# Kernel optimization log

Measured on AMD Instinct MI355X. Metric: run time of the kernel, lower is better.

## Reference

```python
import jax, jax.numpy as jnp
import numpy as np

N = 100000   # num_nodes
E = 3200000  # num_edges (avg degree 32)
T = 16       # channels
L = 2        # n_layers


def setup_inputs() -> dict:
    key = jax.random.key(0)
    ks = jax.random.split(key, 6)
    x = jax.random.normal(ks[0], (T, N), dtype=jnp.float32)
    edge_index = jax.random.randint(ks[1], (2, E), 0, N)
    # per-layer scalar params (shared='all' -> shape [1,1] each), init U(-1,1)
    alpha1 = jax.random.uniform(ks[2], (L, 1, 1), minval=-1.0, maxval=1.0, dtype=jnp.float32)
    alpha2 = jax.random.uniform(ks[3], (L, 1, 1), minval=-1.0, maxval=1.0, dtype=jnp.float32)
    gamma = jax.random.uniform(ks[4], (L, 1, 1), minval=-1.0, maxval=1.0, dtype=jnp.float32)
    bias = jax.random.uniform(ks[5], (L, 1, 1), minval=-1.0, maxval=1.0, dtype=jnp.float32)
    return {"x": x, "edge_index": edge_index, "alpha1": alpha1,
            "alpha2": alpha2, "gamma": gamma, "bias": bias}


def reference(x, edge_index, alpha1, alpha2, gamma, bias):
    # DGMRF forward (transpose=False, with_bias=True): stack of L DGMRFLayerMultiChannel
    src, dst = edge_index[0], edge_index[1]
    # degrees = ptg.utils.degree(edge_index[0]) (out-degree of source nodes)
    deg = jax.ops.segment_sum(jnp.ones(E, dtype=x.dtype), src, num_segments=N)
    log_deg = jnp.log(deg)[None, :]          # [1, N]
    edge_log_deg = log_deg[0, dst][None, :]  # [1, E] = log_degrees[edge_index[1]] (non-transpose)
    for l in range(L):
        dp = jax.nn.sigmoid(gamma[l])        # degree_power, [1,1]
        sw = jnp.exp(alpha1[l])              # self_weight
        # NOTE: source's alpha2 property returns alpha1_param when shared != 'dynamics'
        nw = sw * jnp.tanh(alpha1[l])        # neighbor_weight
        weighted_repr = x * jnp.exp(dp * log_deg)        # [T, N]
        ew = jnp.exp((dp - 1.0) * edge_log_deg)          # [1, E] (base edge_weights are ones)
        msg = x[:, src] * ew                              # gather + weight: [T, E]
        agg = jnp.zeros_like(x).at[:, dst].add(msg)       # scatter-add aggregate
        x = sw * weighted_repr + nw * agg + bias[l]
    return x
```

## Files before the change

kernel.cpp:

```cpp
#include <hip/hip_runtime.h>


#define TCH 16
#define BBITS 8
#define BINW (1 << BBITS)
#define BLK 256
#define SPILL_CAP 65536

__global__ void k_hist(const int* __restrict__ src, const int* __restrict__ dst,
                       int* __restrict__ Hd, int* __restrict__ Hs,
                       int E, int NB, int CHUNK) {
    extern __shared__ int sm[];
    int* cd = sm; int* cs2 = sm + NB;
    for (int i = threadIdx.x; i < 2 * NB; i += blockDim.x) sm[i] = 0;
    __syncthreads();
    int beg = blockIdx.x * CHUNK;
    int end = beg + CHUNK; if (end > E) end = E;
    for (int i = beg + threadIdx.x; i < end; i += blockDim.x) {
        atomicAdd(&cd[dst[i] >> BBITS], 1);
        atomicAdd(&cs2[src[i] >> BBITS], 1);
    }
    __syncthreads();
    int* hd = Hd + (size_t)blockIdx.x * NB;
    int* hs = Hs + (size_t)blockIdx.x * NB;
    for (int b = threadIdx.x; b < NB; b += blockDim.x) { hd[b] = cd[b]; hs[b] = cs2[b]; }
}

__global__ void k_scanb(const int* __restrict__ H, int* __restrict__ off,
                        int* __restrict__ cnt, int NB, int NBLK) {
    __shared__ int ss[BLK];
    int bin = blockIdx.x;
    int t = threadIdx.x;
    int v[4];
    int sum = 0;
#pragma unroll
    for (int j = 0; j < 4; ++j) {
        int b = t * 4 + j;
        v[j] = (b < NBLK) ? H[(size_t)b * NB + bin] : 0;
        sum += v[j];
    }
    ss[t] = sum;
    __syncthreads();
    for (int o = 1; o < BLK; o <<= 1) {
        int u = (t >= o) ? ss[t - o] : 0;
        __syncthreads();
        ss[t] += u;
        __syncthreads();
    }
    int base = ss[t] - sum;
#pragma unroll
    for (int j = 0; j < 4; ++j) {
        int b = t * 4 + j;
        if (b < NBLK) off[(size_t)b * NB + bin] = base;
        base += v[j];
    }
    if (t == BLK - 1) cnt[bin] = ss[BLK - 1];
}

__global__ __launch_bounds__(BLK) void k_place(
        const int* __restrict__ src, const int* __restrict__ dst,
        const int* __restrict__ offd, const int* __restrict__ offs,
        int* __restrict__ dpairs, unsigned char* __restrict__ srcb,
        int* __restrict__ spill_cnt, int* __restrict__ spill_d,
        int* __restrict__ spill_s,
        int E, int NB, int CHUNK, int CAPB) {
    __shared__ int ss[BLK];
    extern __shared__ int sm[];
    int* cur = sm;
    int* gdl = sm + NB;
    int* pay = sm + 2 * NB;
    int* ga  = sm + 2 * NB + CHUNK;

    int t = threadIdx.x;
    int beg = blockIdx.x * CHUNK;
    int end = beg + CHUNK; if (end > E) end = E;
    int m = end - beg;

    for (int i = t; i < NB; i += BLK) cur[i] = 0;
    __syncthreads();
    for (int i = beg + t; i < end; i += BLK)
        atomicAdd(&cur[dst[i] >> BBITS], 1);
    __syncthreads();
    int c0 = (2 * t     < NB) ? cur[2 * t]     : 0;
    int c1 = (2 * t + 1 < NB) ? cur[2 * t + 1] : 0;
    ss[t] = c0 + c1;
    __syncthreads();
    for (int o = 1; o < BLK; o <<= 1) {
        int v = (t >= o) ? ss[t - o] : 0;
        __syncthreads();
        ss[t] += v;
        __syncthreads();
    }
    int excl = ss[t] - (c0 + c1);
    __syncthreads();
    if (2 * t < NB) {
        int od = offd[(size_t)blockIdx.x * NB + 2 * t];
        cur[2 * t] = excl;
        gdl[2 * t] = 2 * t * CAPB + od - excl;
    }
    if (2 * t + 1 < NB) {
        int od = offd[(size_t)blockIdx.x * NB + 2 * t + 1];
        cur[2 * t + 1] = excl + c0;
        gdl[2 * t + 1] = (2 * t + 1) * CAPB + od - (excl + c0);
    }
    __syncthreads();
    for (int i = beg + t; i < end; i += BLK) {
        int d = dst[i], s = src[i];
        int bd = d >> BBITS;
        int ls = atomicAdd(&cur[bd], 1);
        int g  = gdl[bd] + ls;
        if (g < (bd + 1) * CAPB) {
            pay[ls] = ((d & (BINW - 1)) << 24) | s;
            ga[ls] = g;
        } else {
            ga[ls] = -1;
            int p = atomicAdd(&spill_cnt[0], 1);
            if (p < SPILL_CAP) { spill_d[2 * p] = d; spill_d[2 * p + 1] = s; }
        }
    }
    __syncthreads();
    for (int i = t; i < m; i += BLK) {
        int g = ga[i];
        if (g >= 0) dpairs[g] = pay[i];
    }
    __syncthreads();

    unsigned char* payb = (unsigned char*)pay;
    for (int i = t; i < NB; i += BLK) cur[i] = 0;
    __syncthreads();
    for (int i = beg + t; i < end; i += BLK)
        atomicAdd(&cur[src[i] >> BBITS], 1);
    __syncthreads();
    c0 = (2 * t     < NB) ? cur[2 * t]     : 0;
    c1 = (2 * t + 1 < NB) ? cur[2 * t + 1] : 0;
    ss[t] = c0 + c1;
    __syncthreads();
    for (int o = 1; o < BLK; o <<= 1) {
        int v = (t >= o) ? ss[t - o] : 0;
        __syncthreads();
        ss[t] += v;
        __syncthreads();
    }
    excl = ss[t] - (c0 + c1);
    __syncthreads();
    if (2 * t < NB) {
        int os_ = offs[(size_t)blockIdx.x * NB + 2 * t];
        cur[2 * t] = excl;
        gdl[2 * t] = 2 * t * CAPB + os_ - excl;
    }
    if (2 * t + 1 < NB) {
        int os_ = offs[(size_t)blockIdx.x * NB + 2 * t + 1];
        cur[2 * t + 1] = excl + c0;
        gdl[2 * t + 1] = (2 * t + 1) * CAPB + os_ - (excl + c0);
    }
    __syncthreads();
    for (int i = beg + t; i < end; i += BLK) {
        int s = src[i];
        int bs = s >> BBITS;
        int ls = atomicAdd(&cur[bs], 1);
        int g  = gdl[bs] + ls;
        if (g < (bs + 1) * CAPB) {
            payb[ls] = (unsigned char)(s & (BINW - 1));
            ga[ls] = g;
        } else {
            ga[ls] = -1;
            int p = atomicAdd(&spill_cnt[1], 1);
            if (p < SPILL_CAP) spill_s[p] = s;
        }
    }
    __syncthreads();
    for (int i = t; i < m; i += BLK) {
        int g = ga[i];
        if (g >= 0) srcb[g] = payb[i];
    }
}

__global__ void k_binsort(const int* __restrict__ dpairs, const int* __restrict__ cntd,
                          const unsigned char* __restrict__ srcb, const int* __restrict__ cnts,
                          int* __restrict__ adj, int* __restrict__ rptr,
                          int* __restrict__ rcnt, int* __restrict__ deg,
                          int N, int CAPB) {
    __shared__ int h[BINW];
    __shared__ int o[BINW];
    __shared__ int rk[BINW];
    __shared__ int hd[BINW];
    int bin = blockIdx.x;
    int t = threadIdx.x;
    h[t] = 0; rk[t] = 0; hd[t] = 0;
    __syncthreads();
    int m = cntd[bin]; if (m > CAPB) m = CAPB;
    const int* pp = dpairs + (size_t)bin * CAPB;
    for (int i = t; i < m; i += blockDim.x)
        atomicAdd(&h[((unsigned)pp[i]) >> 24], 1);
    int ms = cnts[bin]; if (ms > CAPB) ms = CAPB;
    const unsigned char* sp = srcb + (size_t)bin * CAPB;
    for (int i = t; i < ms; i += blockDim.x)
        atomicAdd(&hd[sp[i]], 1);
    __syncthreads();
    o[t] = h[t];
    __syncthreads();
    for (int s = 1; s < BINW; s <<= 1) {
        int v = 0;
        if (t >= s) v = o[t - s];
        __syncthreads();
        if (t >= s) o[t] += v;
        __syncthreads();
    }
    int binbase = bin * CAPB;
    {
        int excl = o[t] - h[t];
        o[t] = excl;
        int n = (bin << BBITS) + t;
        if (n < N) { rptr[n] = binbase + excl; rcnt[n] = h[t]; deg[n] = hd[t]; }
    }
    __syncthreads();
    for (int i = t; i < m; i += blockDim.x) {
        int w = pp[i];
        int dl = ((unsigned)w) >> 24;
        int s  = w & 0xFFFFFF;
        int r = atomicAdd(&rk[dl], 1);
        adj[binbase + o[dl] + r] = s;
    }
}

__global__ void k_deg_spill(const int* __restrict__ spill_cnt, const int* __restrict__ spill_s,
                            int* __restrict__ deg) {
    int total = spill_cnt[1]; if (total > SPILL_CAP) total = SPILL_CAP;
    int stride = gridDim.x * blockDim.x;
    for (int i = blockIdx.x * blockDim.x + threadIdx.x; i < total; i += stride)
        atomicAdd(&deg[spill_s[i]], 1);
}

__global__ void k_tin(const float* __restrict__ x, float* __restrict__ xt, int N) {
    int n = blockIdx.x * blockDim.x + threadIdx.x;
    if (n >= N) return;
    float v[TCH];
#pragma unroll
    for (int t = 0; t < TCH; ++t) v[t] = x[(size_t)t * N + n];
    float4* o = reinterpret_cast<float4*>(xt + (size_t)n * TCH);
    o[0] = make_float4(v[0],  v[1],  v[2],  v[3]);
    o[1] = make_float4(v[4],  v[5],  v[6],  v[7]);
    o[2] = make_float4(v[8],  v[9],  v[10], v[11]);
    o[3] = make_float4(v[12], v[13], v[14], v[15]);
}

__global__ void k_layer(const float* __restrict__ xin, float* __restrict__ xout,
                        const int* __restrict__ rptr, const int* __restrict__ rcnt,
                        const int* __restrict__ adj, const int* __restrict__ deg,
                        const float* __restrict__ a1p, const float* __restrict__ gp,
                        const float* __restrict__ bp, int l, int N,
                        int last, float* __restrict__ out) {
    int tt = blockIdx.x * blockDim.x + threadIdx.x;
    int n = tt >> 2;
    int q = tt & 3;
    if (n >= N) return;
    float a1 = a1p[l], g = gp[l], bi = bp[l];
    float dp = 1.0f / (1.0f + expf(-g));
    float sw = expf(a1);
    float nw = sw * tanhf(a1);

    int b = rptr[n], m = rcnt[n];
    const int* row = adj + b;
    float4 acc0 = make_float4(0.f, 0.f, 0.f, 0.f);
    float4 acc1 = make_float4(0.f, 0.f, 0.f, 0.f);
    float4 acc2 = make_float4(0.f, 0.f, 0.f, 0.f);
    float4 acc3 = make_float4(0.f, 0.f, 0.f, 0.f);
    int i = 0;
    for (; i + 7 < m; i += 8) {
        int s0 = row[i],     s1 = row[i + 1], s2 = row[i + 2], s3 = row[i + 3];
        int s4 = row[i + 4], s5 = row[i + 5], s6 = row[i + 6], s7 = row[i + 7];
        float4 x0 = reinterpret_cast<const float4*>(xin + (size_t)s0 * TCH)[q];
        float4 x1 = reinterpret_cast<const float4*>(xin + (size_t)s1 * TCH)[q];
        float4 x2 = reinterpret_cast<const float4*>(xin + (size_t)s2 * TCH)[q];
        float4 x3 = reinterpret_cast<const float4*>(xin + (size_t)s3 * TCH)[q];
        float4 x4 = reinterpret_cast<const float4*>(xin + (size_t)s4 * TCH)[q];
        float4 x5 = reinterpret_cast<const float4*>(xin + (size_t)s5 * TCH)[q];
        float4 x6 = reinterpret_cast<const float4*>(xin + (size_t)s6 * TCH)[q];
        float4 x7 = reinterpret_cast<const float4*>(xin + (size_t)s7 * TCH)[q];
        acc0.x += x0.x; acc0.y += x0.y; acc0.z += x0.z; acc0.w += x0.w;
        acc1.x += x1.x; acc1.y += x1.y; acc1.z += x1.z; acc1.w += x1.w;
        acc2.x += x2.x; acc2.y += x2.y; acc2.z += x2.z; acc2.w += x2.w;
        acc3.x += x3.x; acc3.y += x3.y; acc3.z += x3.z; acc3.w += x3.w;
        acc0.x += x4.x; acc0.y += x4.y; acc0.z += x4.z; acc0.w += x4.w;
        acc1.x += x5.x; acc1.y += x5.y; acc1.z += x5.z; acc1.w += x5.w;
        acc2.x += x6.x; acc2.y += x6.y; acc2.z += x6.z; acc2.w += x6.w;
        acc3.x += x7.x; acc3.y += x7.y; acc3.z += x7.z; acc3.w += x7.w;
    }
    for (; i < m; ++i) {
        int s0 = row[i];
        float4 x0 = reinterpret_cast<const float4*>(xin + (size_t)s0 * TCH)[q];
        acc0.x += x0.x; acc0.y += x0.y; acc0.z += x0.z; acc0.w += x0.w;
    }
    acc0.x += acc1.x + acc2.x + acc3.x;
    acc0.y += acc1.y + acc2.y + acc3.y;
    acc0.z += acc1.z + acc2.z + acc3.z;
    acc0.w += acc1.w + acc2.w + acc3.w;

    float ldg = logf((float)deg[n]);
    float cs = sw * expf(dp * ldg);
    float cn = nw * expf((dp - 1.0f) * ldg);

    float4 xq = reinterpret_cast<const float4*>(xin + (size_t)n * TCH)[q];
    float4 r;
    r.x = cs * xq.x + cn * acc0.x + bi;
    r.y = cs * xq.y + cn * acc0.y + bi;
    r.z = cs * xq.z + cn * acc0.z + bi;
    r.w = cs * xq.w + cn * acc0.w + bi;

    if (last) {
        int t0 = q * 4;
        out[(size_t)(t0 + 0) * N + n] = r.x;
        out[(size_t)(t0 + 1) * N + n] = r.y;
        out[(size_t)(t0 + 2) * N + n] = r.z;
        out[(size_t)(t0 + 3) * N + n] = r.w;
    } else {
        reinterpret_cast<float4*>(xout + (size_t)n * TCH)[q] = r;
    }
}

__global__ void k_spill(const int* __restrict__ spill_cnt, const int* __restrict__ spill_d,
                        const float* __restrict__ xin, float* __restrict__ xout,
                        const int* __restrict__ deg,
                        const float* __restrict__ a1p, const float* __restrict__ gp,
                        int l, int N, int last, float* __restrict__ out) {
    int total = spill_cnt[0]; if (total > SPILL_CAP) total = SPILL_CAP;
    int stride = gridDim.x * blockDim.x;
    float a1 = a1p[l], g = gp[l];
    float dp = 1.0f / (1.0f + expf(-g));
    float nw = expf(a1) * tanhf(a1);
    for (int p = blockIdx.x * blockDim.x + threadIdx.x; p < total; p += stride) {
        int d = spill_d[2 * p], s = spill_d[2 * p + 1];
        float cn = nw * expf((dp - 1.0f) * logf((float)deg[d]));
#pragma unroll
        for (int t = 0; t < TCH; ++t) {
            float v = cn * xin[(size_t)s * TCH + t];
            if (last) atomicAdd(&out[(size_t)t * N + d], v);
            else      atomicAdd(&xout[(size_t)d * TCH + t], v);
        }
    }
}

extern "C" void kernel_launch(void* const* d_in, const int* in_sizes, int n_in,
                              void* d_out, int out_size, void* d_ws, size_t ws_size,
                              hipStream_t stream) {
    const float* x      = (const float*)d_in[0];
    const int*   ei     = (const int*)d_in[1];
    const float* alpha1 = (const float*)d_in[2];
    const float* gamma  = (const float*)d_in[4];
    const float* bias   = (const float*)d_in[5];
    float* out = (float*)d_out;

    const int N = in_sizes[0] / TCH;
    const int E = in_sizes[1] / 2;
    const int L = in_sizes[2];
    const int* src = ei;
    const int* dst = ei + E;

    const int NB = (N + BINW - 1) >> BBITS;
    int CHUNK = 4096;
    int NBLK = (E + CHUNK - 1) / CHUNK;
    while (NBLK > 4 * BLK) { CHUNK *= 2; NBLK = (E + CHUNK - 1) / CHUNK; }

    auto align = [](size_t v) { return (v + 255) & ~(size_t)255; };
    char* ws = (char*)d_ws;
    size_t off = 0;
    int* deg     = (int*)(ws + off); off += align((size_t)N * 4);
    int* rptr    = (int*)(ws + off); off += align((size_t)N * 4);
    int* rcnt    = (int*)(ws + off); off += align((size_t)N * 4);
    int* cntd    = (int*)(ws + off); off += align((size_t)NB * 4);
    int* cnts    = (int*)(ws + off); off += align((size_t)NB * 4);
    int* Hd      = (int*)(ws + off); off += align((size_t)NBLK * NB * 4);
    int* Hs      = (int*)(ws + off); off += align((size_t)NBLK * NB * 4);
    int* offd    = (int*)(ws + off); off += align((size_t)NBLK * NB * 4);
    int* offs    = (int*)(ws + off); off += align((size_t)NBLK * NB * 4);
    int* spill_c = (int*)(ws + off); off += 256;
    int* spill_d = (int*)(ws + off); off += align((size_t)SPILL_CAP * 8);
    int* spill_s = (int*)(ws + off); off += align((size_t)SPILL_CAP * 4);
    float* xt0   = (float*)(ws + off); off += align((size_t)N * TCH * 4);
    float* xt1   = (float*)(ws + off); off += align((size_t)N * TCH * 4);
    long long avg = ((long long)E * BINW + N - 1) / N;
    int CAPB = (int)(avg + avg / 16 + 64);
    size_t rem = (ws_size > off) ? (ws_size - off) : 0;
    size_t cap_fit = rem / ((size_t)NB * 9 + 8);
    if ((size_t)CAPB > cap_fit) CAPB = (int)cap_fit;
    if (CAPB < 1) CAPB = 1;
    int* dpairs  = (int*)(ws + off); off += align((size_t)NB * CAPB * 4);
    int* adj     = (int*)(ws + off); off += align((size_t)NB * CAPB * 4);
    unsigned char* srcb = (unsigned char*)(ws + off);

    dim3 b(BLK), gN((N + BLK - 1) / BLK);
    dim3 gN4(((size_t)N * 4 + BLK - 1) / BLK);

    size_t place_lds = ((size_t)2 * NB + 2 * CHUNK) * 4;

    hipMemsetAsync(spill_c, 0, 256, stream);
    k_hist   <<<dim3(NBLK), b, 2 * NB * 4, stream>>>(src, dst, Hd, Hs, E, NB, CHUNK);
    k_scanb  <<<dim3(NB),   b, 0,          stream>>>(Hd, offd, cntd, NB, NBLK);
    k_scanb  <<<dim3(NB),   b, 0,          stream>>>(Hs, offs, cnts, NB, NBLK);
    k_place  <<<dim3(NBLK), b, place_lds,  stream>>>(src, dst, offd, offs, dpairs, srcb,
                                                     spill_c, spill_d, spill_s,
                                                     E, NB, CHUNK, CAPB);
    k_binsort<<<dim3(NB),   b, 0,          stream>>>(dpairs, cntd, srcb, cnts,
                                                     adj, rptr, rcnt, deg, N, CAPB);
    k_deg_spill<<<dim3(16), b, 0,          stream>>>(spill_c, spill_s, deg);
    k_tin    <<<gN,         b, 0,          stream>>>(x, xt0, N);

    float* xin = xt0;
    float* xo  = xt1;
    for (int l = 0; l < L; ++l) {
        int last = (l == L - 1) ? 1 : 0;
        k_layer<<<gN4, b, 0, stream>>>(xin, xo, rptr, rcnt, adj, deg,
                                       alpha1, gamma, bias, l, N, last, out);
        k_spill<<<dim3(16), b, 0, stream>>>(spill_c, spill_d, xin, xo, deg,
                                            alpha1, gamma, l, N, last, out);
        float* tmp = xin; xin = xo; xo = tmp;
    }
}
```

Measured before the change: 198.4 us.

## Split features into channel halves, stage binsort in LDS, scan in place

Features are stored as two 8-channel planes, and each layer runs two passes, one per half. Each gathered row is then 32 bytes, so the working set per pass is half as large and should fit better in cache. The bin sort now scatters into LDS and writes adjacency rows out contiguously. The scan writes offsets back in place, which removes the separate offset buffers. Chunk size is halved, with a cap on CAPB so the LDS size stays bounded, and the adjacency and row-pointer reads use nontemporal loads. The cost is that adjacency indices are read twice per layer, and two launches per layer add overhead.

After: 257.8 us. +29.9%, slower.

```diff
diff --git a/kernel.cpp b/kernel.cpp
--- a/kernel.cpp
+++ b/kernel.cpp
@@ -2,6 +2,7 @@
 
 
 #define TCH 16
+#define HCH 8
 #define BBITS 8
 #define BINW (1 << BBITS)
 #define BLK 256
@@ -26,16 +27,16 @@
     for (int b = threadIdx.x; b < NB; b += blockDim.x) { hd[b] = cd[b]; hs[b] = cs2[b]; }
 }
 
-__global__ void k_scanb(const int* __restrict__ H, int* __restrict__ off,
-                        int* __restrict__ cnt, int NB, int NBLK) {
+__global__ void k_scanb(int* __restrict__ H, int* __restrict__ cnt,
+                        int NB, int NBLK) {
     __shared__ int ss[BLK];
     int bin = blockIdx.x;
     int t = threadIdx.x;
-    int v[4];
+    int v[8];
     int sum = 0;
 #pragma unroll
-    for (int j = 0; j < 4; ++j) {
-        int b = t * 4 + j;
+    for (int j = 0; j < 8; ++j) {
+        int b = t * 8 + j;
         v[j] = (b < NBLK) ? H[(size_t)b * NB + bin] : 0;
         sum += v[j];
     }
@@ -49,9 +50,9 @@
     }
     int base = ss[t] - sum;
 #pragma unroll
-    for (int j = 0; j < 4; ++j) {
-        int b = t * 4 + j;
-        if (b < NBLK) off[(size_t)b * NB + bin] = base;
+    for (int j = 0; j < 8; ++j) {
+        int b = t * 8 + j;
+        if (b < NBLK) H[(size_t)b * NB + bin] = base;
         base += v[j];
     }
     if (t == BLK - 1) cnt[bin] = ss[BLK - 1];
@@ -175,26 +176,28 @@
     }
 }
 
-__global__ void k_binsort(const int* __restrict__ dpairs, const int* __restrict__ cntd,
-                          const unsigned char* __restrict__ srcb, const int* __restrict__ cnts,
-                          int* __restrict__ adj, int* __restrict__ rptr,
-                          int* __restrict__ rcnt, int* __restrict__ deg,
-                          int N, int CAPB) {
+__global__ __launch_bounds__(BLK) void k_binsort(
+        const int* __restrict__ dpairs, const int* __restrict__ cntd,
+        const unsigned char* __restrict__ srcb, const int* __restrict__ cnts,
+        int* __restrict__ adj, int* __restrict__ rptr,
+        int* __restrict__ rcnt, int* __restrict__ deg,
+        int N, int CAPB) {
     __shared__ int h[BINW];
     __shared__ int o[BINW];
     __shared__ int rk[BINW];
     __shared__ int hd[BINW];
+    extern __shared__ int lbuf[];
     int bin = blockIdx.x;
     int t = threadIdx.x;
     h[t] = 0; rk[t] = 0; hd[t] = 0;
     __syncthreads();
     int m = cntd[bin]; if (m > CAPB) m = CAPB;
     const int* pp = dpairs + (size_t)bin * CAPB;
-    for (int i = t; i < m; i += blockDim.x)
+    for (int i = t; i < m; i += BLK)
         atomicAdd(&h[((unsigned)pp[i]) >> 24], 1);
     int ms = cnts[bin]; if (ms > CAPB) ms = CAPB;
     const unsigned char* sp = srcb + (size_t)bin * CAPB;
-    for (int i = t; i < ms; i += blockDim.x)
+    for (int i = t; i < ms; i += BLK)
         atomicAdd(&hd[sp[i]], 1);
     __syncthreads();
     o[t] = h[t];
@@ -214,13 +217,16 @@
         if (n < N) { rptr[n] = binbase + excl; rcnt[n] = h[t]; deg[n] = hd[t]; }
     }
     __syncthreads();
-    for (int i = t; i < m; i += blockDim.x) {
+    for (int i = t; i < m; i += BLK) {
         int w = pp[i];
         int dl = ((unsigned)w) >> 24;
         int s  = w & 0xFFFFFF;
         int r = atomicAdd(&rk[dl], 1);
-        adj[binbase + o[dl] + r] = s;
-    }
+        lbuf[o[dl] + r] = s;
+    }
+    __syncthreads();
+    for (int i = t; i < m; i += BLK)
+        adj[binbase + i] = lbuf[i];
 }
 
 __global__ void k_deg_spill(const int* __restrict__ spill_cnt, const int* __restrict__ spill_s,
@@ -237,29 +243,32 @@
     float v[TCH];
 #pragma unroll
     for (int t = 0; t < TCH; ++t) v[t] = x[(size_t)t * N + n];
-    float4* o = reinterpret_cast<float4*>(xt + (size_t)n * TCH);
-    o[0] = make_float4(v[0],  v[1],  v[2],  v[3]);
-    o[1] = make_float4(v[4],  v[5],  v[6],  v[7]);
-    o[2] = make_float4(v[8],  v[9],  v[10], v[11]);
-    o[3] = make_float4(v[12], v[13], v[14], v[15]);
+    float4* h0 = reinterpret_cast<float4*>(xt + (size_t)n * HCH);
+    float4* h1 = reinterpret_cast<float4*>(xt + (size_t)N * HCH + (size_t)n * HCH);
+    h0[0] = make_float4(v[0],  v[1],  v[2],  v[3]);
+    h0[1] = make_float4(v[4],  v[5],  v[6],  v[7]);
+    h1[0] = make_float4(v[8],  v[9],  v[10], v[11]);
+    h1[1] = make_float4(v[12], v[13], v[14], v[15]);
 }
 
 __global__ void k_layer(const float* __restrict__ xin, float* __restrict__ xout,
                         const int* __restrict__ rptr, const int* __restrict__ rcnt,
                         const int* __restrict__ adj, const int* __restrict__ deg,
                         const float* __restrict__ a1p, const float* __restrict__ gp,
-                        const float* __restrict__ bp, int l, int N,
+                        const float* __restrict__ bp, int l, int N, int half,
                         int last, float* __restrict__ out) {
     int tt = blockIdx.x * blockDim.x + threadIdx.x;
-    int n = tt >> 2;
-    int q = tt & 3;
+    int n = tt >> 1;
+    int q = tt & 1;
     if (n >= N) return;
+    const float* xh = xin + (size_t)half * N * HCH;
     float a1 = a1p[l], g = gp[l], bi = bp[l];
     float dp = 1.0f / (1.0f + expf(-g));
     float sw = expf(a1);
     float nw = sw * tanhf(a1);
 
-    int b = rptr[n], m = rcnt[n];
+    int b = __builtin_nontemporal_load(rptr + n);
+    int m = __builtin_nontemporal_load(rcnt + n);
     const int* row = adj + b;
     float4 acc0 = make_float4(0.f, 0.f, 0.f, 0.f);
     float4 acc1 = make_float4(0.f, 0.f, 0.f, 0.f);
@@ -267,16 +276,22 @@
     float4 acc3 = make_float4(0.f, 0.f, 0.f, 0.f);
     int i = 0;
     for (; i + 7 < m; i += 8) {
-        int s0 = row[i],     s1 = row[i + 1], s2 = row[i + 2], s3 = row[i + 3];
-        int s4 = row[i + 4], s5 = row[i + 5], s6 = row[i + 6], s7 = row[i + 7];
-        float4 x0 = reinterpret_cast<const float4*>(xin + (size_t)s0 * TCH)[q];
-        float4 x1 = reinterpret_cast<const float4*>(xin + (size_t)s1 * TCH)[q];
-        float4 x2 = reinterpret_cast<const float4*>(xin + (size_t)s2 * TCH)[q];
-        float4 x3 = reinterpret_cast<const float4*>(xin + (size_t)s3 * TCH)[q];
-        float4 x4 = reinterpret_cast<const float4*>(xin + (size_t)s4 * TCH)[q];
-        float4 x5 = reinterpret_cast<const float4*>(xin + (size_t)s5 * TCH)[q];
-        float4 x6 = reinterpret_cast<const float4*>(xin + (size_t)s6 * TCH)[q];
-        float4 x7 = reinterpret_cast<const float4*>(xin + (size_t)s7 * TCH)[q];
+        int s0 = __builtin_nontemporal_load(row + i);
+        int s1 = __builtin_nontemporal_load(row + i + 1);
+        int s2 = __builtin_nontemporal_load(row + i + 2);
+        int s3 = __builtin_nontemporal_load(row + i + 3);
+        int s4 = __builtin_nontemporal_load(row + i + 4);
+        int s5 = __builtin_nontemporal_load(row + i + 5);
+        int s6 = __builtin_nontemporal_load(row + i + 6);
+        int s7 = __builtin_nontemporal_load(row + i + 7);
+        float4 x0 = reinterpret_cast<const float4*>(xh + (size_t)s0 * HCH)[q];
+        float4 x1 = reinterpret_cast<const float4*>(xh + (size_t)s1 * HCH)[q];
+        float4 x2 = reinterpret_cast<const float4*>(xh + (size_t)s2 * HCH)[q];
+        float4 x3 = reinterpret_cast<const float4*>(xh + (size_t)s3 * HCH)[q];
+        float4 x4 = reinterpret_cast<const float4*>(xh + (size_t)s4 * HCH)[q];
+        float4 x5 = reinterpret_cast<const float4*>(xh + (size_t)s5 * HCH)[q];
+        float4 x6 = reinterpret_cast<const float4*>(xh + (size_t)s6 * HCH)[q];
+        float4 x7 = reinterpret_cast<const float4*>(xh + (size_t)s7 * HCH)[q];
         acc0.x += x0.x; acc0.y += x0.y; acc0.z += x0.z; acc0.w += x0.w;
         acc1.x += x1.x; acc1.y += x1.y; acc1.z += x1.z; acc1.w += x1.w;
         acc2.x += x2.x; acc2.y += x2.y; acc2.z += x2.z; acc2.w += x2.w;
@@ -287,8 +302,8 @@
         acc3.x += x7.x; acc3.y += x7.y; acc3.z += x7.z; acc3.w += x7.w;
     }
     for (; i < m; ++i) {
-        int s0 = row[i];
-        float4 x0 = reinterpret_cast<const float4*>(xin + (size_t)s0 * TCH)[q];
+        int s0 = __builtin_nontemporal_load(row + i);
+        float4 x0 = reinterpret_cast<const float4*>(xh + (size_t)s0 * HCH)[q];
         acc0.x += x0.x; acc0.y += x0.y; acc0.z += x0.z; acc0.w += x0.w;
     }
     acc0.x += acc1.x + acc2.x + acc3.x;
@@ -300,7 +315,7 @@
     float cs = sw * expf(dp * ldg);
     float cn = nw * expf((dp - 1.0f) * ldg);
 
-    float4 xq = reinterpret_cast<const float4*>(xin + (size_t)n * TCH)[q];
+    float4 xq = reinterpret_cast<const float4*>(xh + (size_t)n * HCH)[q];
     float4 r;
     r.x = cs * xq.x + cn * acc0.x + bi;
     r.y = cs * xq.y + cn * acc0.y + bi;
@@ -308,13 +323,13 @@
     r.w = cs * xq.w + cn * acc0.w + bi;
 
     if (last) {
-        int t0 = q * 4;
+        int t0 = half * HCH + q * 4;
         out[(size_t)(t0 + 0) * N + n] = r.x;
         out[(size_t)(t0 + 1) * N + n] = r.y;
         out[(size_t)(t0 + 2) * N + n] = r.z;
         out[(size_t)(t0 + 3) * N + n] = r.w;
     } else {
-        reinterpret_cast<float4*>(xout + (size_t)n * TCH)[q] = r;
+        reinterpret_cast<float4*>(xout + (size_t)half * N * HCH + (size_t)n * HCH)[q] = r;
     }
 }
 
@@ -333,9 +348,10 @@
         float cn = nw * expf((dp - 1.0f) * logf((float)deg[d]));
 #pragma unroll
         for (int t = 0; t < TCH; ++t) {
-            float v = cn * xin[(size_t)s * TCH + t];
+            int half = t >> 3, c = t & 7;
+            float v = cn * xin[(size_t)half * N * HCH + (size_t)s * HCH + c];
             if (last) atomicAdd(&out[(size_t)t * N + d], v);
-            else      atomicAdd(&xout[(size_t)d * TCH + t], v);
+            else      atomicAdd(&xout[(size_t)half * N * HCH + (size_t)d * HCH + c], v);
         }
     }
 }
@@ -357,9 +373,9 @@
     const int* dst = ei + E;
 
     const int NB = (N + BINW - 1) >> BBITS;
-    int CHUNK = 4096;
+    int CHUNK = 2048;
     int NBLK = (E + CHUNK - 1) / CHUNK;
-    while (NBLK > 4 * BLK) { CHUNK *= 2; NBLK = (E + CHUNK - 1) / CHUNK; }
+    while (NBLK > 8 * BLK) { CHUNK *= 2; NBLK = (E + CHUNK - 1) / CHUNK; }
 
     auto align = [](size_t v) { return (v + 255) & ~(size_t)255; };
     char* ws = (char*)d_ws;
@@ -371,8 +387,6 @@
     int* cnts    = (int*)(ws + off); off += align((size_t)NB * 4);
     int* Hd      = (int*)(ws + off); off += align((size_t)NBLK * NB * 4);
     int* Hs      = (int*)(ws + off); off += align((size_t)NBLK * NB * 4);
-    int* offd    = (int*)(ws + off); off += align((size_t)NBLK * NB * 4);
-    int* offs    = (int*)(ws + off); off += align((size_t)NBLK * NB * 4);
     int* spill_c = (int*)(ws + off); off += 256;
     int* spill_d = (int*)(ws + off); off += align((size_t)SPILL_CAP * 8);
     int* spill_s = (int*)(ws + off); off += align((size_t)SPILL_CAP * 4);
@@ -384,33 +398,38 @@
     size_t cap_fit = rem / ((size_t)NB * 9 + 8);
     if ((size_t)CAPB > cap_fit) CAPB = (int)cap_fit;
     if (CAPB < 1) CAPB = 1;
+    if (CAPB > 30000) CAPB = 30000;
     int* dpairs  = (int*)(ws + off); off += align((size_t)NB * CAPB * 4);
     int* adj     = (int*)(ws + off); off += align((size_t)NB * CAPB * 4);
     unsigned char* srcb = (unsigned char*)(ws + off);
 
     dim3 b(BLK), gN((N + BLK - 1) / BLK);
-    dim3 gN4(((size_t)N * 4 + BLK - 1) / BLK);
-
+    dim3 gN2(((size_t)N * 2 + BLK - 1) / BLK);
+
+    size_t hist_lds  = (size_t)2 * NB * 4;
     size_t place_lds = ((size_t)2 * NB + 2 * CHUNK) * 4;
+    size_t sort_lds  = (size_t)CAPB * 4;
 
     hipMemsetAsync(spill_c, 0, 256, stream);
-    k_hist   <<<dim3(NBLK), b, 2 * NB * 4, stream>>>(src, dst, Hd, Hs, E, NB, CHUNK);
-    k_scanb  <<<dim3(NB),   b, 0,          stream>>>(Hd, offd, cntd, NB, NBLK);
-    k_scanb  <<<dim3(NB),   b, 0,          stream>>>(Hs, offs, cnts, NB, NBLK);
-    k_place  <<<dim3(NBLK), b, place_lds,  stream>>>(src, dst, offd, offs, dpairs, srcb,
-                                                     spill_c, spill_d, spill_s,
-                                                     E, NB, CHUNK, CAPB);
-    k_binsort<<<dim3(NB),   b, 0,          stream>>>(dpairs, cntd, srcb, cnts,
-                                                     adj, rptr, rcnt, deg, N, CAPB);
-    k_deg_spill<<<dim3(16), b, 0,          stream>>>(spill_c, spill_s, deg);
-    k_tin    <<<gN,         b, 0,          stream>>>(x, xt0, N);
+    k_hist   <<<dim3(NBLK), b, hist_lds,  stream>>>(src, dst, Hd, Hs, E, NB, CHUNK);
+    k_scanb  <<<dim3(NB),   b, 0,         stream>>>(Hd, cntd, NB, NBLK);
+    k_scanb  <<<dim3(NB),   b, 0,         stream>>>(Hs, cnts, NB, NBLK);
+    k_place  <<<dim3(NBLK), b, place_lds, stream>>>(src, dst, Hd, Hs, dpairs, srcb,
+                                                    spill_c, spill_d, spill_s,
+                                                    E, NB, CHUNK, CAPB);
+    k_binsort<<<dim3(NB),   b, sort_lds,  stream>>>(dpairs, cntd, srcb, cnts,
+                                                    adj, rptr, rcnt, deg, N, CAPB);
+    k_deg_spill<<<dim3(16), b, 0,         stream>>>(spill_c, spill_s, deg);
+    k_tin    <<<gN,         b, 0,         stream>>>(x, xt0, N);
 
     float* xin = xt0;
     float* xo  = xt1;
     for (int l = 0; l < L; ++l) {
         int last = (l == L - 1) ? 1 : 0;
-        k_layer<<<gN4, b, 0, stream>>>(xin, xo, rptr, rcnt, adj, deg,
-                                       alpha1, gamma, bias, l, N, last, out);
+        k_layer<<<gN2, b, 0, stream>>>(xin, xo, rptr, rcnt, adj, deg,
+                                       alpha1, gamma, bias, l, N, 0, last, out);
+        k_layer<<<gN2, b, 0, stream>>>(xin, xo, rptr, rcnt, adj, deg,
+                                       alpha1, gamma, bias, l, N, 1, last, out);
         k_spill<<<dim3(16), b, 0, stream>>>(spill_c, spill_d, xin, xo, deg,
                                             alpha1, gamma, l, N, last, out);
         float* tmp = xin; xin = xo; xo = tmp;
```
